# Kernel optimization log

Hardware: AMD Instinct MI355X
Metric: run time of the kernel (lower is better)

## Reference

```python
import jax, jax.numpy as jnp
import numpy as np

B, C, N, T = 32, 32, 512, 168
EMB = 40
K_NEI = 20
ALPHA = 3.0          # saturation rate in graph learning
GCN_DEPTH = 2
PROP_ALPHA = 0.05    # retaining ratio in mix-hop propagation
KERNELS = (2, 3, 6, 7)
DIL = 2
T_OUT = T - (max(KERNELS) - 1) * DIL   # 156
C_BR = C // len(KERNELS)               # 8 channels per inception branch
EPS = 1e-5


def _conv2d(x, w, b, dil):
    # x: (B,Cin,N,T), w: (Cout,Cin,1,k), temporal dilation dil
    y = jax.lax.conv_general_dilated(
        x, w, window_strides=(1, 1), padding='VALID',
        rhs_dilation=(1, dil), dimension_numbers=('NCHW', 'OIHW', 'NCHW'))
    return y + b[None, :, None, None]


def _inception(x, ws, bs):
    outs = [_conv2d(x, w, b, DIL) for w, b in zip(ws, bs)]
    tmin = outs[-1].shape[-1]   # largest kernel -> shortest output
    return jnp.concatenate([o[..., -tmin:] for o in outs], axis=1)


def setup_inputs() -> dict:
    key = jax.random.key(0)
    ks = jax.random.split(key, 32)
    d = {}
    d['x'] = jax.random.normal(ks[0], (B, C, N, T), jnp.float32)
    d['idx'] = jnp.arange(N)  # permutation of nodes (identity)
    # graph learning params
    d['emb1'] = jax.random.normal(ks[1], (N, EMB), jnp.float32)
    d['emb2'] = jax.random.normal(ks[2], (N, EMB), jnp.float32)
    d['W1'] = jax.random.normal(ks[3], (EMB, EMB), jnp.float32) * 0.15
    d['b1'] = jnp.zeros((EMB,), jnp.float32)
    d['W2'] = jax.random.normal(ks[4], (EMB, EMB), jnp.float32) * 0.15
    d['b2'] = jnp.zeros((EMB,), jnp.float32)
    # dilated inception filter/gate conv params
    i = 5
    for pre in ('f', 'g'):
        for k in KERNELS:
            d[f'{pre}w{k}'] = jax.random.normal(ks[i], (C_BR, C, 1, k), jnp.float32) * 0.05
            d[f'{pre}b{k}'] = jnp.zeros((C_BR,), jnp.float32)
            i += 1
    # mix-hop 1x1 mlp: (gcn_depth+1)*C -> C
    d['mlp_w'] = jax.random.normal(ks[i], (C, (GCN_DEPTH + 1) * C, 1, 1), jnp.float32) * 0.05
    d['mlp_b'] = jnp.zeros((C,), jnp.float32)
    # node-indexed layer norm affine params, shape (C, N, T_OUT)
    d['ln_w'] = jnp.ones((C, N, T_OUT), jnp.float32)
    d['ln_b'] = jnp.zeros((C, N, T_OUT), jnp.float32)
    return d


def reference(x, idx, emb1, emb2, W1, b1, W2, b2,
              fw2, fb2, fw3, fb3, fw6, fb6, fw7, fb7,
              gw2, gb2, gw3, gb3, gw6, gb6, gw7, gb7,
              mlp_w, mlp_b, ln_w, ln_b):
    # ---- graph learning: topk-masked adjacency (N,N) ----
    n1 = jnp.tanh(ALPHA * (emb1[idx] @ W1.T + b1))
    n2 = jnp.tanh(ALPHA * (emb2[idx] @ W2.T + b2))
    a = n1 @ n2.T - n2 @ n1.T
    A = jax.nn.relu(jnp.tanh(ALPHA * a))
    _, top_idx = jax.lax.top_k(A, K_NEI)                 # deterministic topk (torch adds rand*0.01 tiebreak)
    mask = jnp.zeros_like(A).at[jnp.arange(A.shape[0])[:, None], top_idx].set(1.0)
    A = A * mask

    # ---- dilated inception gated temporal conv ----
    filt = jnp.tanh(_inception(x, (fw2, fw3, fw6, fw7), (fb2, fb3, fb6, fb7)))
    gate = jax.nn.sigmoid(_inception(x, (gw2, gw3, gw6, gw7), (gb2, gb3, gb6, gb7)))
    z = filt * gate                                       # (B, C, N, T_OUT)

    # ---- mix-hop graph convolution ----
    Ah = A + jnp.eye(A.shape[0], dtype=A.dtype)
    Ah = Ah / Ah.sum(1, keepdims=True)                    # row-degree normalization
    h = z
    hops = [z]
    for _ in range(GCN_DEPTH):
        h = PROP_ALPHA * z + (1.0 - PROP_ALPHA) * jnp.einsum('bcwt,vw->bcvt', h, Ah)
        hops.append(h)
    h0 = jnp.concatenate(hops, axis=1)                    # (B, 3C, N, T_OUT)
    out = _conv2d(h0, mlp_w, mlp_b, 1)                    # 1x1 mlp -> (B, C, N, T_OUT)

    # ---- residual + node-indexed layer norm over dims (C,N,T) ----
    out = out + x[..., -T_OUT:]
    mean = out.mean(axis=(1, 2, 3), keepdims=True)
    var = out.var(axis=(1, 2, 3), keepdims=True)
    out = (out - mean) * jax.lax.rsqrt(var + EPS)
    out = out * ln_w[:, idx, :][None] + ln_b[:, idx, :][None]
    return out
```

## Files before the change

### kernel.cpp

```cpp
#include <hip/hip_runtime.h>

#define NB 32
#define NC 32
#define NNODE 512
#define NT 168
#define NTO 156
#define NQ 39
#define NEMB 40
#define KNEI 20
#define NADJ 21
#define ZT_PITCH 42
#define XROWS 176
#define NPB 4
#define CT (NC * NTO)
#define NPAIR (CT / 8)

static_assert(NTO == 4 * NQ, "t quads");

typedef __attribute__((ext_vector_type(8))) short bf16x8;
typedef __attribute__((ext_vector_type(16))) float f32x16;
typedef __attribute__((ext_vector_type(4))) float f32x4;
typedef __attribute__((ext_vector_type(8))) unsigned short u16x8;
typedef __attribute__((ext_vector_type(4))) unsigned short u16x4;

__device__ __forceinline__ float fast_tanh(float x) {
  float e = __expf(2.0f * x);
  return 1.0f - 2.0f / (e + 1.0f);
}
__device__ __forceinline__ float fast_sigmoid(float x) {
  return 1.0f / (1.0f + __expf(-x));
}
__device__ __forceinline__ unsigned short f2b(float v) {
  unsigned int u = __float_as_uint(v);
  unsigned int r = (u + 0x7FFFu + ((u >> 16) & 1u)) >> 16;
  return (unsigned short)r;
}
__device__ __forceinline__ float b2f(unsigned short u) {
  return __uint_as_float((unsigned int)u << 16);
}
template <typename T>
__device__ __forceinline__ void pin(T& v) {
  f32x4 t = __builtin_bit_cast(f32x4, v);
  asm volatile("" : "+v"(t));
  v = __builtin_bit_cast(T, t);
}

__global__ __launch_bounds__(128) void g1_kernel(
    const float* __restrict__ emb1, const float* __restrict__ emb2,
    const float* __restrict__ W1, const float* __restrict__ b1,
    const float* __restrict__ W2, const float* __restrict__ b2,
    const int* __restrict__ idx, float* __restrict__ n1, float* __restrict__ n2) {
  const int v = blockIdx.x;
  const int tid = threadIdx.x;
  const int iv = idx[v];
  if (tid < NEMB) {
    float s = b1[tid];
    const float* er = emb1 + iv * NEMB;
    const float* wr = W1 + tid * NEMB;
    for (int f = 0; f < NEMB; ++f) s = fmaf(er[f], wr[f], s);
    n1[v * NEMB + tid] = tanhf(3.0f * s);
  } else if (tid >= 64 && tid < 64 + NEMB) {
    const int e = tid - 64;
    float s = b2[e];
    const float* er = emb2 + iv * NEMB;
    const float* wr = W2 + e * NEMB;
    for (int f = 0; f < NEMB; ++f) s = fmaf(er[f], wr[f], s);
    n2[v * NEMB + e] = tanhf(3.0f * s);
  }
}

__global__ __launch_bounds__(256) void g2_kernel(
    const float* __restrict__ n1, const float* __restrict__ n2,
    int* __restrict__ cols, float* __restrict__ wts) {
  const int v = blockIdx.x;
  const int tid = threadIdx.x;
  volatile __shared__ float Arow[NNODE];
  __shared__ float n1v[NEMB], n2v[NEMB];
  if (tid < NEMB) n1v[tid] = n1[v * NEMB + tid];
  if (tid >= 64 && tid < 64 + NEMB) n2v[tid - 64] = n2[v * NEMB + tid - 64];
  __syncthreads();
  for (int w = tid; w < NNODE; w += 256) {
    float d1 = 0.f, d2 = 0.f;
    const float* r1 = n1 + w * NEMB;
    const float* r2 = n2 + w * NEMB;
    for (int e = 0; e < NEMB; ++e) {
      d1 = fmaf(n1v[e], r2[e], d1);
      d2 = fmaf(n2v[e], r1[e], d2);
    }
    float a = tanhf(3.0f * (d1 - d2));
    Arow[w] = a > 0.f ? a : 0.f;
  }
  __syncthreads();
  if (tid >= 64) return;
  float sum = 1.0f;
  float selv[KNEI];
  int seli[KNEI];
  #pragma unroll
  for (int s = 0; s < KNEI; ++s) {
    float bv = -1.f; int bi = NNODE;
    #pragma unroll
    for (int w8 = 0; w8 < NNODE / 64; ++w8) {
      const int w = tid + 64 * w8;
      const float val = Arow[w];
      if (val > bv || (val == bv && w < bi)) { bv = val; bi = w; }
    }
    #pragma unroll
    for (int off = 32; off >= 1; off >>= 1) {
      const float ov = __shfl_down(bv, off);
      const int oi = __shfl_down(bi, off);
      if (ov > bv || (ov == bv && oi < bi)) { bv = ov; bi = oi; }
    }
    bv = __shfl(bv, 0);
    bi = __shfl(bi, 0);
    selv[s] = bv;
    seli[s] = bi;
    Arow[bi] = -2.f;
    sum += bv;
  }
  if (tid == 0) {
    const float inv = 1.0f / sum;
    #pragma unroll
    for (int s = 0; s < KNEI; ++s) {
      cols[v * NADJ + s] = seli[s];
      wts[v * NADJ + s] = selv[s] * inv;
    }
    cols[v * NADJ + KNEI] = v;
    wts[v * NADJ + KNEI] = inv;
  }
}

struct ZParams {
  const float* fw[4]; const float* fb[4];
  const float* gw[4]; const float* gb[4];
};

#define PA_CNT (2 * 2 * 7 * 64 * 8)
#define PB_CNT (2 * 64 * 16)
#define PNA_CNT (3 * 2 * 64 * 8)
__global__ __launch_bounds__(256) void pack_kernel(ZParams p, const float* __restrict__ mw,
                                                   unsigned short* __restrict__ pA,
                                                   float* __restrict__ pB,
                                                   unsigned short* __restrict__ pNA) {
  const int idx = blockIdx.x * 256 + threadIdx.x;
  if (idx < PA_CNT) {
    const int e = idx & 7;
    const int l = (idx >> 3) & 63;
    int rest = idx >> 9;
    const int j = rest % 7;
    rest /= 7;
    const int s = rest & 1;
    const int m = rest >> 1;
    const int row = l & 31;
    const int k = ((l >> 5) << 3) + e;
    const int ci = s * 16 + k;
    const int isF = (row < 16);
    const int co = m * 16 + (isF ? row : row - 16);
    const int br = co >> 3;
    const int kk = (br == 0) ? 2 : (br == 1) ? 3 : (br == 2) ? 6 : 7;
    const int jw = j - (7 - kk);
    const float* arr = isF ? p.fw[br] : p.gw[br];
    float val = (jw >= 0) ? arr[((co & 7) * NC + ci) * kk + jw] : 0.f;
    pA[idx] = f2b(val);
  } else if (idx < PA_CNT + PB_CNT) {
    const int ib = idx - PA_CNT;
    const int r = ib & 15;
    const int l = (ib >> 4) & 63;
    const int m = ib >> 10;
    const int rr = r & 7;
    const int row = (rr & 3) + 8 * (rr >> 2) + 4 * (l >> 5);
    const int co = m * 16 + row;
    const int br = co >> 3;
    const float* arr = (r < 8) ? p.fb[br] : p.gb[br];
    pB[ib] = arr[co & 7];
  } else if (idx < PA_CNT + PB_CNT + PNA_CNT) {
    const int in_ = idx - (PA_CNT + PB_CNT);
    const int e = in_ & 7;
    const int l = (in_ >> 3) & 63;
    const int s = (in_ >> 9) & 1;
    const int which = in_ >> 10;
    const int co = l & 31;
    const int c = s * 16 + ((l >> 5) << 3) + e;
    const float w0 = mw[co * 96 + c];
    const float w1 = mw[co * 96 + 32 + c];
    const float w2 = mw[co * 96 + 64 + c];
    float val;
    if (which == 0)      val = w0 + 0.05f * (w1 + w2);
    else if (which == 1) val = 0.95f * w1 + 0.0475f * w2;
    else                 val = 0.9025f * w2;
    pNA[in_] = f2b(val);
  }
}

__global__ __launch_bounds__(256) void xprep_kernel(
    const float* __restrict__ x, unsigned short* __restrict__ xbf) {
  const int n = blockIdx.x;
  const int b = blockIdx.y;
  const int tid = threadIdx.x;
  const int cp = tid & 15;
  const int t0 = tid >> 4;
  const float* xc0 = x + ((size_t)(b * NC + 2 * cp) * NNODE + n) * NT;
  const float* xc1 = xc0 + (size_t)NNODE * NT;
  unsigned int* dst = (unsigned int*)(xbf + (size_t)(b * NNODE + n) * (XROWS * NC));
  #pragma unroll
  for (int k = 0; k < 11; ++k) {
    const int t = t0 + 16 * k;
    unsigned int v = 0;
    if (t < NT) {
      v = (unsigned int)f2b(xc0[t]) | ((unsigned int)f2b(xc1[t]) << 16);
    }
    dst[t * 16 + cp] = v;
  }
}

__attribute__((amdgpu_waves_per_eu(2)))
__global__ __launch_bounds__(256) void conv_kernel(
    const unsigned short* __restrict__ xbf, const unsigned short* __restrict__ pA,
    const float* __restrict__ pBias, unsigned short* __restrict__ z) {
  __shared__ unsigned short zt0[NTO * ZT_PITCH];
  __shared__ unsigned short zt1[NTO * ZT_PITCH];
  const int n0 = blockIdx.x * NPB;
  const int b = blockIdx.y;
  const int tid = threadIdx.x;
  const int w = tid >> 6, l = tid & 63;
  const int jc = l & 31, h = l >> 5;
  const int m = w & 1;

  bf16x8 aF[2][7];
  #pragma unroll
  for (int s = 0; s < 2; ++s)
    #pragma unroll
    for (int j = 0; j < 7; ++j) {
      aF[s][j] = *reinterpret_cast<const bf16x8*>(
          pA + ((((m * 2 + s) * 7 + j) << 6) + l) * 8);
      pin(aF[s][j]);
    }
  f32x4 bias4[4];
  {
    const f32x4* pb4 = reinterpret_cast<const f32x4*>(pBias + (m * 64 + l) * 16);
    #pragma unroll
    for (int q = 0; q < 4; ++q) { bias4[q] = pb4[q]; pin(bias4[q]); }
  }

  #pragma unroll
  for (int nn = 0; nn < NPB; ++nn) {
    const int n = n0 + nn;
    unsigned short* zt = (nn & 1) ? zt1 : zt0;
    const unsigned short* xbn = xbf + (size_t)(b * NNODE + n) * (XROWS * NC);
    for (int tile = (w >> 1); tile < 5; tile += 2) {
      const int t0 = tile * 32;
      f32x16 acc;
      #pragma unroll
      for (int r = 0; r < 16; ++r) acc[r] = bias4[r >> 2][r & 3];
      const unsigned short* bp = xbn + (t0 + jc) * NC + h * 8;
      #pragma unroll
      for (int j = 0; j < 7; ++j) {
        bf16x8 b0 = *reinterpret_cast<const bf16x8*>(bp + 2 * j * NC);
        bf16x8 b1 = *reinterpret_cast<const bf16x8*>(bp + 2 * j * NC + 16);
        acc = __builtin_amdgcn_mfma_f32_32x32x16_bf16(aF[0][j], b0, acc, 0, 0, 0);
        acc = __builtin_amdgcn_mfma_f32_32x32x16_bf16(aF[1][j], b1, acc, 0, 0, 0);
      }
      const int t = t0 + jc;
      if (t < NTO) {
        #pragma unroll
        for (int r = 0; r < 8; ++r) {
          const float f = fast_tanh(acc[r]);
          const float g = fast_sigmoid(acc[r + 8]);
          const int row = (r & 3) + 8 * (r >> 2) + 4 * h;
          const int co = m * 16 + row;
          zt[t * ZT_PITCH + co] = f2b(f * g);
        }
      }
    }
    __syncthreads();
    unsigned short* zv = z + (size_t)(b * NNODE + n) * CT;
    for (int i = tid; i < CT / 4; i += 256) {
      const int row = i >> 3, q = i & 7;
      ushort4 v4 = *reinterpret_cast<const ushort4*>(zt + row * ZT_PITCH + 4 * q);
      *reinterpret_cast<ushort4*>(zv + 4 * i) = v4;
    }
  }
}

__global__ __launch_bounds__(256) void hop_kernel(
    const unsigned short* __restrict__ src, const int* __restrict__ cols,
    const float* __restrict__ wts, unsigned short* __restrict__ dst) {
  const int bid = blockIdx.x;
  const int r = bid & 7;
  const int t_ = bid >> 3;
  const int v = t_ & (NNODE - 1);
  const int g = t_ >> 9;
  const int b = g * 8 + r;
  const int tid = threadIdx.x;
  float acc[3][8];
  #pragma unroll
  for (int k = 0; k < 3; ++k)
    #pragma unroll
    for (int j = 0; j < 8; ++j) acc[k][j] = 0.f;
  for (int s = 0; s < NADJ; ++s) {
    const int col = cols[v * NADJ + s];
    const float w = wts[v * NADJ + s];
    const unsigned short* p = src + ((size_t)(b << 9) + col) * CT;
    #pragma unroll
    for (int k = 0; k < 2; ++k) {
      u16x8 u = *reinterpret_cast<const u16x8*>(p + 8 * (tid + 256 * k));
      #pragma unroll
      for (int j = 0; j < 8; ++j) acc[k][j] = fmaf(w, b2f(u[j]), acc[k][j]);
    }
    if (tid < NPAIR - 512) {
      u16x8 u = *reinterpret_cast<const u16x8*>(p + 8 * (tid + 512));
      #pragma unroll
      for (int j = 0; j < 8; ++j) acc[2][j] = fmaf(w, b2f(u[j]), acc[2][j]);
    }
  }
  unsigned short* dp = dst + ((size_t)(b << 9) + v) * CT;
  #pragma unroll
  for (int k = 0; k < 2; ++k) {
    u16x8 o;
    #pragma unroll
    for (int j = 0; j < 8; ++j) o[j] = f2b(acc[k][j]);
    *reinterpret_cast<u16x8*>(dp + 8 * (tid + 256 * k)) = o;
  }
  if (tid < NPAIR - 512) {
    u16x8 o;
    #pragma unroll
    for (int j = 0; j < 8; ++j) o[j] = f2b(acc[2][j]);
    *reinterpret_cast<u16x8*>(dp + 8 * (tid + 512)) = o;
  }
}

__global__ __launch_bounds__(256) void fin_kernel(
    const unsigned short* __restrict__ z, const unsigned short* __restrict__ g1,
    const unsigned short* __restrict__ g2, const unsigned short* __restrict__ xbf,
    const unsigned short* __restrict__ pNA, const float* __restrict__ mb,
    unsigned short* __restrict__ P, float* __restrict__ stats) {
  const int b = blockIdx.y;
  const int tid = threadIdx.x;
  const int w = tid >> 6, l = tid & 63;
  const int jc = l & 31, h = l >> 5;
  const int v = blockIdx.x * 4 + w;

  bf16x8 nA[3][2];
  #pragma unroll
  for (int which = 0; which < 3; ++which)
    #pragma unroll
    for (int s = 0; s < 2; ++s) {
      nA[which][s] = *reinterpret_cast<const bf16x8*>(
          pNA + (((which * 2 + s) << 6) + l) * 8);
      pin(nA[which][s]);
    }
  float mbr[16];
  #pragma unroll
  for (int r = 0; r < 16; ++r) {
    const int co = (r & 3) + 8 * (r >> 2) + 4 * h;
    mbr[r] = mb[co];
  }

  const size_t base = (size_t)(b << 9) + v;
  const unsigned short* zs_ = z + base * CT;
  const unsigned short* g1s = g1 + base * CT;
  const unsigned short* g2s = g2 + base * CT;
  const unsigned short* xres = xbf + (size_t)(b * NNODE + v) * (XROWS * NC) + 12 * NC;
  unsigned short* Ps = P + base * CT;
  float st1 = 0.f, st2 = 0.f;

  #pragma unroll
  for (int tile = 0; tile < 5; ++tile) {
    const int t = tile * 32 + jc;
    const int off = t * NC + h * 8;
    f32x16 acc;
    #pragma unroll
    for (int r = 0; r < 16; ++r) acc[r] = 0.f;
    {
      bf16x8 b0 = *reinterpret_cast<const bf16x8*>(zs_ + off);
      bf16x8 b1 = *reinterpret_cast<const bf16x8*>(zs_ + off + 16);
      acc = __builtin_amdgcn_mfma_f32_32x32x16_bf16(nA[0][0], b0, acc, 0, 0, 0);
      acc = __builtin_amdgcn_mfma_f32_32x32x16_bf16(nA[0][1], b1, acc, 0, 0, 0);
    }
    {
      bf16x8 b0 = *reinterpret_cast<const bf16x8*>(g1s + off);
      bf16x8 b1 = *reinterpret_cast<const bf16x8*>(g1s + off + 16);
      acc = __builtin_amdgcn_mfma_f32_32x32x16_bf16(nA[1][0], b0, acc, 0, 0, 0);
      acc = __builtin_amdgcn_mfma_f32_32x32x16_bf16(nA[1][1], b1, acc, 0, 0, 0);
    }
    {
      bf16x8 b0 = *reinterpret_cast<const bf16x8*>(g2s + off);
      bf16x8 b1 = *reinterpret_cast<const bf16x8*>(g2s + off + 16);
      acc = __builtin_amdgcn_mfma_f32_32x32x16_bf16(nA[2][0], b0, acc, 0, 0, 0);
      acc = __builtin_amdgcn_mfma_f32_32x32x16_bf16(nA[2][1], b1, acc, 0, 0, 0);
    }
    if (t < NTO) {
      u16x4 xu[4];
      #pragma unroll
      for (int g = 0; g < 4; ++g)
        xu[g] = *reinterpret_cast<const u16x4*>(xres + t * NC + 4 * h + 8 * g);
      #pragma unroll
      for (int r = 0; r < 16; ++r) {
        const int co = (r & 3) + 8 * (r >> 2) + 4 * h;
        const float xr = b2f(xu[r >> 2][r & 3]);
        const float val = acc[r] + mbr[r] + xr;
        Ps[co * NTO + t] = f2b(val);
        st1 += val;
        st2 += val * val;
      }
    }
  }
  #pragma unroll
  for (int off = 32; off >= 1; off >>= 1) {
    st1 += __shfl_down(st1, off);
    st2 += __shfl_down(st2, off);
  }
  __shared__ float r1[4], r2[4];
  if ((tid & 63) == 0) { r1[w] = st1; r2[w] = st2; }
  __syncthreads();
  if (tid == 0) {
    atomicAdd(&stats[b * 2], r1[0] + r1[1] + r1[2] + r1[3]);
    atomicAdd(&stats[b * 2 + 1], r2[0] + r2[1] + r2[2] + r2[3]);
  }
}

__global__ __launch_bounds__(256) void ln_kernel(
    const unsigned short* __restrict__ P, float* __restrict__ out,
    const float* __restrict__ lnw, const float* __restrict__ lnb,
    const int* __restrict__ idx, const float* __restrict__ stats) {
  const int i = blockIdx.x * 256 + threadIdx.x;
  const int q = i % NQ;
  const int r = i / NQ;
  const int co = r % NC;
  const int v = r / NC;
  const int iv = idx[v];
  const int lb = (co * NNODE + iv) * NTO + 4 * q;
  const float4 w = *reinterpret_cast<const float4*>(lnw + lb);
  const float4 bb = *reinterpret_cast<const float4*>(lnb + lb);
  const float invM = 1.0f / (float)(NC * NNODE * NTO);
  const int poff = (v * NC + co) * NTO + 4 * q;
  const int ooff = (co * NNODE + v) * NTO + 4 * q;
  for (int b = 0; b < NB; ++b) {
    const float mean = stats[b * 2] * invM;
    const float var = stats[b * 2 + 1] * invM - mean * mean;
    const float rs = rsqrtf(var + 1e-5f);
    ushort4 u = *reinterpret_cast<const ushort4*>(P + (size_t)b * (NNODE * CT) + poff);
    float4 o;
    o.x = (b2f(u.x) - mean) * rs * w.x + bb.x;
    o.y = (b2f(u.y) - mean) * rs * w.y + bb.y;
    o.z = (b2f(u.z) - mean) * rs * w.z + bb.z;
    o.w = (b2f(u.w) - mean) * rs * w.w + bb.w;
    *reinterpret_cast<float4*>(out + (size_t)b * (NC * NNODE * NTO) + ooff) = o;
  }
}

extern "C" void kernel_launch(void* const* d_in, const int* in_sizes, int n_in,
                              void* d_out, int out_size, void* d_ws, size_t ws_size,
                              hipStream_t stream) {
  const float* x    = (const float*)d_in[0];
  const int*   idx  = (const int*)d_in[1];
  const float* emb1 = (const float*)d_in[2];
  const float* emb2 = (const float*)d_in[3];
  const float* W1   = (const float*)d_in[4];
  const float* b1   = (const float*)d_in[5];
  const float* W2   = (const float*)d_in[6];
  const float* b2   = (const float*)d_in[7];
  const float* mlp_w = (const float*)d_in[24];
  const float* mlp_b = (const float*)d_in[25];
  const float* ln_w = (const float*)d_in[26];
  const float* ln_b = (const float*)d_in[27];

  char* ws = (char*)d_ws;
  float* n1    = (float*)(ws);
  float* n2    = (float*)(ws + (128 << 10));
  int*   cols  = (int*)  (ws + (256 << 10));
  float* wts   = (float*)(ws + (320 << 10));
  float* stats = (float*)(ws + (384 << 10));
  unsigned short* pA = (unsigned short*)(ws + (400 << 10));
  float* pBias = (float*)(ws + (440 << 10));
  unsigned short* pNA = (unsigned short*)(ws + (456 << 10));
  unsigned short* xbf = (unsigned short*)(ws + (512 << 10));
  const size_t xbf_elems = (size_t)NB * NNODE * XROWS * NC;
  const size_t slab_elems = (size_t)NB * NNODE * CT;
  unsigned short* z  = xbf + xbf_elems;
  unsigned short* g1 = z + slab_elems;
  unsigned short* g2 = g1 + slab_elems;
  unsigned short* P  = g2 + slab_elems;

  ZParams zp;
  for (int k = 0; k < 4; ++k) {
    zp.fw[k] = (const float*)d_in[8 + 2 * k];
    zp.fb[k] = (const float*)d_in[9 + 2 * k];
    zp.gw[k] = (const float*)d_in[16 + 2 * k];
    zp.gb[k] = (const float*)d_in[17 + 2 * k];
  }

  hipMemsetAsync(stats, 0, 2 * NB * sizeof(float), stream);
  g1_kernel<<<NNODE, 128, 0, stream>>>(emb1, emb2, W1, b1, W2, b2, idx, n1, n2);
  g2_kernel<<<NNODE, 256, 0, stream>>>(n1, n2, cols, wts);
  pack_kernel<<<76, 256, 0, stream>>>(zp, mlp_w, pA, pBias, pNA);
  xprep_kernel<<<dim3(NNODE, NB), 256, 0, stream>>>(x, xbf);
  conv_kernel<<<dim3(NNODE / NPB, NB), 256, 0, stream>>>(xbf, pA, pBias, z);
  hop_kernel<<<NB * NNODE, 256, 0, stream>>>(z, cols, wts, g1);
  hop_kernel<<<NB * NNODE, 256, 0, stream>>>(g1, cols, wts, g2);
  fin_kernel<<<dim3(NNODE / 4, NB), 256, 0, stream>>>(z, g1, g2, xbf, pNA, mlp_b,
                                                      P, stats);
  ln_kernel<<<NNODE * NC * NQ / 256, 256, 0, stream>>>(P, (float*)d_out, ln_w,
                                                       ln_b, idx, stats);
}
```

Baseline: 1.204 ms.

## Fuse second graph hop into final MLP kernel, keeping hop output in LDS

The second neighbour-aggregation hop moves into the final 1x1-MLP/residual kernel. Each block now handles one node, gathers the neighbour rows of g1, and writes the result to shared memory, where the MFMA stage reads it directly. This drops one kernel launch and the full global write and re-read of the g2 buffer. The cost is a four-times larger grid with one node per block, an uneven split of 5 tiles across 4 waves, and extra LDS use per block.

```diff
diff --git a/kernel.cpp b/kernel.cpp
--- a/kernel.cpp
+++ b/kernel.cpp
@@ -14,6 +14,7 @@
 #define NPB 4
 #define CT (NC * NTO)
 #define NPAIR (CT / 8)
+#define G2P 36
 
 static_assert(NTO == 4 * NQ, "t quads");
 
@@ -328,17 +329,56 @@
   }
 }
 
-__global__ __launch_bounds__(256) void fin_kernel(
+__global__ __launch_bounds__(256) void hf_kernel(
     const unsigned short* __restrict__ z, const unsigned short* __restrict__ g1,
-    const unsigned short* __restrict__ g2, const unsigned short* __restrict__ xbf,
-    const unsigned short* __restrict__ pNA, const float* __restrict__ mb,
-    unsigned short* __restrict__ P, float* __restrict__ stats) {
+    const unsigned short* __restrict__ xbf, const int* __restrict__ cols,
+    const float* __restrict__ wts, const unsigned short* __restrict__ pNA,
+    const float* __restrict__ mb, unsigned short* __restrict__ P,
+    float* __restrict__ stats) {
+  __shared__ unsigned short g2t[160 * G2P];
+  const int v = blockIdx.x;
   const int b = blockIdx.y;
   const int tid = threadIdx.x;
+  if (tid < 4 * G2P) g2t[156 * G2P + tid] = 0;
+
+  {
+    float acc[3][8];
+    #pragma unroll
+    for (int k = 0; k < 3; ++k)
+      #pragma unroll
+      for (int j = 0; j < 8; ++j) acc[k][j] = 0.f;
+    for (int s = 0; s < NADJ; ++s) {
+      const int col = cols[v * NADJ + s];
+      const float w = wts[v * NADJ + s];
+      const unsigned short* p = g1 + ((size_t)(b << 9) + col) * CT;
+      #pragma unroll
+      for (int k = 0; k < 2; ++k) {
+        u16x8 u = *reinterpret_cast<const u16x8*>(p + 8 * (tid + 256 * k));
+        #pragma unroll
+        for (int j = 0; j < 8; ++j) acc[k][j] = fmaf(w, b2f(u[j]), acc[k][j]);
+      }
+      if (tid < NPAIR - 512) {
+        u16x8 u = *reinterpret_cast<const u16x8*>(p + 8 * (tid + 512));
+        #pragma unroll
+        for (int j = 0; j < 8; ++j) acc[2][j] = fmaf(w, b2f(u[j]), acc[2][j]);
+      }
+    }
+    #pragma unroll
+    for (int k = 0; k < 3; ++k) {
+      const int pi = tid + 256 * k;
+      if (pi < NPAIR) {
+        const int t = pi >> 2, g = pi & 3;
+        u16x8 o;
+        #pragma unroll
+        for (int j = 0; j < 8; ++j) o[j] = f2b(acc[k][j]);
+        *reinterpret_cast<u16x8*>(g2t + t * G2P + 8 * g) = o;
+      }
+    }
+  }
+  __syncthreads();
+
   const int w = tid >> 6, l = tid & 63;
   const int jc = l & 31, h = l >> 5;
-  const int v = blockIdx.x * 4 + w;
-
   bf16x8 nA[3][2];
   #pragma unroll
   for (int which = 0; which < 3; ++which)
@@ -354,19 +394,17 @@
     const int co = (r & 3) + 8 * (r >> 2) + 4 * h;
     mbr[r] = mb[co];
   }
-
   const size_t base = (size_t)(b << 9) + v;
   const unsigned short* zs_ = z + base * CT;
   const unsigned short* g1s = g1 + base * CT;
-  const unsigned short* g2s = g2 + base * CT;
   const unsigned short* xres = xbf + (size_t)(b * NNODE + v) * (XROWS * NC) + 12 * NC;
   unsigned short* Ps = P + base * CT;
   float st1 = 0.f, st2 = 0.f;
 
-  #pragma unroll
-  for (int tile = 0; tile < 5; ++tile) {
+  for (int tile = w; tile < 5; tile += 4) {
     const int t = tile * 32 + jc;
     const int off = t * NC + h * 8;
+    const unsigned short* lp = g2t + t * G2P + h * 8;
     f32x16 acc;
     #pragma unroll
     for (int r = 0; r < 16; ++r) acc[r] = 0.f;
@@ -383,8 +421,8 @@
       acc = __builtin_amdgcn_mfma_f32_32x32x16_bf16(nA[1][1], b1, acc, 0, 0, 0);
     }
     {
-      bf16x8 b0 = *reinterpret_cast<const bf16x8*>(g2s + off);
-      bf16x8 b1 = *reinterpret_cast<const bf16x8*>(g2s + off + 16);
+      bf16x8 b0 = *reinterpret_cast<const bf16x8*>(lp);
+      bf16x8 b1 = *reinterpret_cast<const bf16x8*>(lp + 16);
       acc = __builtin_amdgcn_mfma_f32_32x32x16_bf16(nA[2][0], b0, acc, 0, 0, 0);
       acc = __builtin_amdgcn_mfma_f32_32x32x16_bf16(nA[2][1], b1, acc, 0, 0, 0);
     }
@@ -478,8 +516,7 @@
   const size_t slab_elems = (size_t)NB * NNODE * CT;
   unsigned short* z  = xbf + xbf_elems;
   unsigned short* g1 = z + slab_elems;
-  unsigned short* g2 = g1 + slab_elems;
-  unsigned short* P  = g2 + slab_elems;
+  unsigned short* P  = g1 + slab_elems;
 
   ZParams zp;
   for (int k = 0; k < 4; ++k) {
@@ -496,9 +533,8 @@
   xprep_kernel<<<dim3(NNODE, NB), 256, 0, stream>>>(x, xbf);
   conv_kernel<<<dim3(NNODE / NPB, NB), 256, 0, stream>>>(xbf, pA, pBias, z);
   hop_kernel<<<NB * NNODE, 256, 0, stream>>>(z, cols, wts, g1);
-  hop_kernel<<<NB * NNODE, 256, 0, stream>>>(g1, cols, wts, g2);
-  fin_kernel<<<dim3(NNODE / 4, NB), 256, 0, stream>>>(z, g1, g2, xbf, pNA, mlp_b,
-                                                      P, stats);
+  hf_kernel<<<dim3(NNODE, NB), 256, 0, stream>>>(z, g1, xbf, cols, wts, pNA,
+                                                 mlp_b, P, stats);
   ln_kernel<<<NNODE * NC * NQ / 256, 256, 0, stream>>>(P, (float*)d_out, ln_w,
                                                        ln_b, idx, stats);
 }
```

Result: no change. 1.207 ms (+0.3%).

## Fuse second graph-hop propagation into the final MLP kernel

Applied to the files above, without the earlier changes.

The second hop_kernel launch and the g2 intermediate buffer are removed. The final 1x1-MLP kernel now gathers the 21 weighted neighbour rows of g1 itself, accumulates them in fp32 and converts to bf16 as the third MFMA operand. The goal is to avoid writing and re-reading a full bf16 activation slab through global memory. In exchange, the gather loop now runs inside the MFMA kernel, which adds latency and register pressure per tile.

```diff
diff --git a/kernel.cpp b/kernel.cpp
--- a/kernel.cpp
+++ b/kernel.cpp
@@ -328,14 +328,16 @@
   }
 }
 
-__global__ __launch_bounds__(256) void fin_kernel(
+__global__ __launch_bounds__(256) void hf_kernel(
     const unsigned short* __restrict__ z, const unsigned short* __restrict__ g1,
-    const unsigned short* __restrict__ g2, const unsigned short* __restrict__ xbf,
-    const unsigned short* __restrict__ pNA, const float* __restrict__ mb,
-    unsigned short* __restrict__ P, float* __restrict__ stats) {
+    const unsigned short* __restrict__ xbf, const int* __restrict__ cols,
+    const float* __restrict__ wts, const unsigned short* __restrict__ pNA,
+    const float* __restrict__ mb, unsigned short* __restrict__ P,
+    float* __restrict__ stats) {
   const int b = blockIdx.y;
   const int tid = threadIdx.x;
-  const int w = tid >> 6, l = tid & 63;
+  const int w = __builtin_amdgcn_readfirstlane(tid >> 6);
+  const int l = tid & 63;
   const int jc = l & 31, h = l >> 5;
   const int v = blockIdx.x * 4 + w;
 
@@ -358,8 +360,10 @@
   const size_t base = (size_t)(b << 9) + v;
   const unsigned short* zs_ = z + base * CT;
   const unsigned short* g1s = g1 + base * CT;
-  const unsigned short* g2s = g2 + base * CT;
+  const unsigned short* g1b = g1 + ((size_t)(b << 9)) * CT;
   const unsigned short* xres = xbf + (size_t)(b * NNODE + v) * (XROWS * NC) + 12 * NC;
+  const int* cv = cols + v * NADJ;
+  const float* wv = wts + v * NADJ;
   unsigned short* Ps = P + base * CT;
   float st1 = 0.f, st2 = 0.f;
 
@@ -367,6 +371,24 @@
   for (int tile = 0; tile < 5; ++tile) {
     const int t = tile * 32 + jc;
     const int off = t * NC + h * 8;
+    float ag0[8], ag1[8];
+    #pragma unroll
+    for (int j = 0; j < 8; ++j) { ag0[j] = 0.f; ag1[j] = 0.f; }
+    for (int s = 0; s < NADJ; ++s) {
+      const int col = cv[s];
+      const float wt = wv[s];
+      const unsigned short* p = g1b + (size_t)col * CT + off;
+      u16x8 ua = *reinterpret_cast<const u16x8*>(p);
+      u16x8 ub = *reinterpret_cast<const u16x8*>(p + 16);
+      #pragma unroll
+      for (int j = 0; j < 8; ++j) {
+        ag0[j] = fmaf(wt, b2f(ua[j]), ag0[j]);
+        ag1[j] = fmaf(wt, b2f(ub[j]), ag1[j]);
+      }
+    }
+    u16x8 gb0, gb1;
+    #pragma unroll
+    for (int j = 0; j < 8; ++j) { gb0[j] = f2b(ag0[j]); gb1[j] = f2b(ag1[j]); }
     f32x16 acc;
     #pragma unroll
     for (int r = 0; r < 16; ++r) acc[r] = 0.f;
@@ -382,12 +404,10 @@
       acc = __builtin_amdgcn_mfma_f32_32x32x16_bf16(nA[1][0], b0, acc, 0, 0, 0);
       acc = __builtin_amdgcn_mfma_f32_32x32x16_bf16(nA[1][1], b1, acc, 0, 0, 0);
     }
-    {
-      bf16x8 b0 = *reinterpret_cast<const bf16x8*>(g2s + off);
-      bf16x8 b1 = *reinterpret_cast<const bf16x8*>(g2s + off + 16);
-      acc = __builtin_amdgcn_mfma_f32_32x32x16_bf16(nA[2][0], b0, acc, 0, 0, 0);
-      acc = __builtin_amdgcn_mfma_f32_32x32x16_bf16(nA[2][1], b1, acc, 0, 0, 0);
-    }
+    acc = __builtin_amdgcn_mfma_f32_32x32x16_bf16(
+        nA[2][0], __builtin_bit_cast(bf16x8, gb0), acc, 0, 0, 0);
+    acc = __builtin_amdgcn_mfma_f32_32x32x16_bf16(
+        nA[2][1], __builtin_bit_cast(bf16x8, gb1), acc, 0, 0, 0);
     if (t < NTO) {
       u16x4 xu[4];
       #pragma unroll
@@ -478,8 +498,7 @@
   const size_t slab_elems = (size_t)NB * NNODE * CT;
   unsigned short* z  = xbf + xbf_elems;
   unsigned short* g1 = z + slab_elems;
-  unsigned short* g2 = g1 + slab_elems;
-  unsigned short* P  = g2 + slab_elems;
+  unsigned short* P  = g1 + slab_elems;
 
   ZParams zp;
   for (int k = 0; k < 4; ++k) {
@@ -496,9 +515,8 @@
   xprep_kernel<<<dim3(NNODE, NB), 256, 0, stream>>>(x, xbf);
   conv_kernel<<<dim3(NNODE / NPB, NB), 256, 0, stream>>>(xbf, pA, pBias, z);
   hop_kernel<<<NB * NNODE, 256, 0, stream>>>(z, cols, wts, g1);
-  hop_kernel<<<NB * NNODE, 256, 0, stream>>>(g1, cols, wts, g2);
-  fin_kernel<<<dim3(NNODE / 4, NB), 256, 0, stream>>>(z, g1, g2, xbf, pNA, mlp_b,
-                                                      P, stats);
+  hf_kernel<<<dim3(NNODE / 4, NB), 256, 0, stream>>>(z, g1, xbf, cols, wts, pNA,
+                                                     mlp_b, P, stats);
   ln_kernel<<<NNODE * NC * NQ / 256, 256, 0, stream>>>(P, (float*)d_out, ln_w,
                                                        ln_b, idx, stats);
 }
```

Measured after the change: 1.303 ms. +8.2%, slower.
